# Kernel tuning notes

Measured on AMD Instinct MI355X. Metric: run time of the kernel, lower is better.

## Reference

```python
import jax, jax.numpy as jnp
import numpy as np

N_MET = 100000
N_RXN = 200000
E_SUB = 400000
E_PROD = 400000
HIDDEN = 128
MSG_DIM = 64
DT = 0.01  # flux-limited Euler step


def setup_inputs() -> dict:
    key = jax.random.key(0)
    ks = jax.random.split(key, 16)
    inp = {
        "x": jax.random.uniform(ks[0], (N_MET, 8), dtype=jnp.float32),
        "met_sub": jax.random.randint(ks[1], (E_SUB,), 0, N_MET, dtype=jnp.int32),
        "rxn_sub": jax.random.randint(ks[2], (E_SUB,), 0, N_RXN, dtype=jnp.int32),
        "sto_sub": jax.random.uniform(ks[3], (E_SUB,), dtype=jnp.float32) + 0.5,
        "met_prod": jax.random.randint(ks[4], (E_PROD,), 0, N_MET, dtype=jnp.int32),
        "rxn_prod": jax.random.randint(ks[5], (E_PROD,), 0, N_RXN, dtype=jnp.int32),
        "sto_prod": jax.random.uniform(ks[6], (E_PROD,), dtype=jnp.float32) + 0.5,
        # msg_mlp: Linear(2->HIDDEN), Tanh, Linear(HIDDEN->MSG_DIM)
        "W1": jax.random.normal(ks[7], (2, HIDDEN), dtype=jnp.float32) * 0.5,
        "b1": jnp.zeros((HIDDEN,), dtype=jnp.float32),
        "W2": jax.random.normal(ks[8], (HIDDEN, MSG_DIM), dtype=jnp.float32) * (1.0 / np.sqrt(HIDDEN)),
        "b2": jnp.zeros((MSG_DIM,), dtype=jnp.float32),
        # rate_mlp: Linear(MSG_DIM->HIDDEN), Tanh, Linear(HIDDEN->1)
        "V1": jax.random.normal(ks[9], (MSG_DIM, HIDDEN), dtype=jnp.float32) * (1.0 / np.sqrt(MSG_DIM)),
        "c1": jnp.zeros((HIDDEN,), dtype=jnp.float32),
        "V2": jax.random.normal(ks[10], (HIDDEN, 1), dtype=jnp.float32) * (1.0 / np.sqrt(HIDDEN)),
        "c2": jnp.zeros((1,), dtype=jnp.float32),
        # log_k ~ U(-2, 1)
        "log_k": jax.random.uniform(ks[11], (N_RXN,), dtype=jnp.float32, minval=-2.0, maxval=1.0),
    }
    return inp


def reference(x, met_sub, rxn_sub, sto_sub, met_prod, rxn_prod, sto_prod,
              W1, b1, W2, b2, V1, c1, V2, c2, log_k):
    n_met = x.shape[0]
    n_rxn = log_k.shape[0]
    conc = x[:, 3]          # [n_met]
    ext = x[:, 4]           # [n_met]

    # gather substrate concentrations -> per-edge msg MLP
    x_src = conc[met_sub]                                   # [E_sub]
    msg_in = jnp.stack([x_src, sto_sub], axis=-1)           # [E_sub, 2]
    h = jnp.tanh(msg_in @ W1 + b1)                          # [E_sub, HIDDEN]
    msg = h @ W2 + b2                                       # [E_sub, MSG_DIM]

    # scatter-add into per-reaction accumulators
    h_rxn = jax.ops.segment_sum(msg, rxn_sub, num_segments=n_rxn)  # [n_rxn, MSG_DIM]

    k = jnp.power(10.0, log_k)                              # [n_rxn]
    base_v = jax.nn.softplus((jnp.tanh(h_rxn @ V1 + c1) @ V2 + c2)[:, 0])  # [n_rxn]

    # multiplicative_substrate modulation: mean external input over substrates
    ones_e = jnp.ones_like(sto_sub)
    n_sub_per_rxn = jnp.clip(jax.ops.segment_sum(ones_e, rxn_sub, num_segments=n_rxn), 1.0)
    ext_agg = jax.ops.segment_sum(ext[met_sub], rxn_sub, num_segments=n_rxn)
    ext_mean = ext_agg / n_sub_per_rxn
    v = k * ext_mean * base_v                               # [n_rxn]

    # flux limiting (dt > 0): no substrate over-consumed in one Euler step
    consumption = sto_sub * v[rxn_sub] * DT                 # [E_sub]
    total_consumption = jax.ops.segment_sum(consumption, met_sub, num_segments=n_met)
    active = total_consumption > 1e-12
    safe_tot = jnp.where(active, total_consumption, 1.0)
    met_scale = jnp.where(active, jnp.minimum(conc / safe_tot, 1.0), 1.0)
    edge_scale = met_scale[met_sub]
    rxn_scale = jnp.ones((n_rxn,), dtype=v.dtype).at[rxn_sub].min(edge_scale)
    v = v * rxn_scale

    # scatter stoichiometric contributions back to metabolites
    met_all = jnp.concatenate([met_sub, met_prod])
    rxn_all = jnp.concatenate([rxn_sub, rxn_prod])
    sto_all = jnp.concatenate([-sto_sub, sto_prod])         # substrates negative, products positive
    contrib = sto_all * v[rxn_all]                          # [E_all]
    dxdt = jax.ops.segment_sum(contrib, met_all, num_segments=n_met)
    return dxdt[:, None]                                    # [n_met, 1]
```

## Files before the change

### kernel.cpp

```cpp
#include <hip/hip_runtime.h>
#include <hip/hip_fp16.h>
#include <cmath>
#include <cstdint>

#define N_MET   100000
#define N_RXN   200000
#define E_SUB   400000
#define E_PROD  400000
#define HIDDEN  128
#define MSG_DIM 64
#define DT      0.01f
#define TGRID   16
#define TGP     17
#define NPTS    (TGP * TGP)
#define CCH     16
#define RPB     128
#define RSB     512
#define NGRP    ((N_RXN + RPB - 1) / RPB)
#define CAP     8
#define OVFMAX  4096
#define NBS8    ((E_SUB / 8 + 255) / 256)
#define PBLK    ((E_PROD + RSB * 4 - 1) / (RSB * 4))
#define STK     10

typedef _Float16 h2v __attribute__((ext_vector_type(2)));

__device__ __forceinline__ float dot2f(uint32_t a, uint32_t b, float c) {
#if __has_builtin(__builtin_amdgcn_fdot2)
    return __builtin_amdgcn_fdot2(__builtin_bit_cast(h2v, a),
                                  __builtin_bit_cast(h2v, b), c, false);
#else
    float2 fa = __half22float2(*(__half2*)&a);
    float2 fb = __half22float2(*(__half2*)&b);
    return fmaf(fa.x, fb.x, fmaf(fa.y, fb.y, c));
#endif
}

__device__ __forceinline__ float fast_tanh(float x) {
    float t = __expf(2.0f * x);
    return 1.0f - 2.0f * __builtin_amdgcn_rcpf(t + 1.0f);
}

__device__ __forceinline__ float softplus_f(float x) {
    return (x > 20.0f) ? x : log1pf(__expf(x));
}

__global__ void __launch_bounds__(256)
prep_all(const float* __restrict__ W1, const float* __restrict__ b1,
         const float* __restrict__ W2, const float* __restrict__ b2,
         const float* __restrict__ V1, __half* __restrict__ TGh,
         const int* __restrict__ rxn_sub, const int* __restrict__ met_sub,
         const float* __restrict__ sto_sub, const float* __restrict__ x,
         int* __restrict__ cnt,
         uint4* __restrict__ recs,
         uint4* __restrict__ ovf, uint2* __restrict__ ovf2,
         int* __restrict__ ovf_cnt) {
    __shared__ float h_s[HIDDEN];
    __shared__ float msg_s[MSG_DIM];
    int bid = blockIdx.x;
    int tid = threadIdx.x;
    if (bid < NPTS) {
        int p = bid;
        int ia = p / TGP, ib = p % TGP;
        float a = (float)ia * (1.0f / TGRID);
        float b = 0.5f + (float)ib * (1.0f / TGRID);
        if (tid < HIDDEN)
            h_s[tid] = tanhf(fmaf(a, W1[tid], fmaf(b, W1[HIDDEN + tid], b1[tid])));
        __syncthreads();
        if (tid < MSG_DIM) {
            float acc = b2[tid];
            #pragma unroll 4
            for (int j = 0; j < HIDDEN; ++j)
                acc = fmaf(h_s[j], W2[j * MSG_DIM + tid], acc);
            msg_s[tid] = acc;
        }
        __syncthreads();
        if (tid < HIDDEN) {
            float g = 0.0f;
            #pragma unroll 4
            for (int m = 0; m < MSG_DIM; ++m)
                g = fmaf(msg_s[m], V1[m * HIDDEN + tid], g);
            int c = tid >> 3;
            int h = tid & 7;
            TGh[((size_t)(c * NPTS + p) * 8) + h] = __float2half(g);
        }
        return;
    }
    int i8 = (bid - NPTS) * 256 + tid;
    if (i8 >= E_SUB / 8) return;
    int4   rr0 = ((const int4*)rxn_sub)[2 * i8],     rr1 = ((const int4*)rxn_sub)[2 * i8 + 1];
    int4   mm0 = ((const int4*)met_sub)[2 * i8],     mm1 = ((const int4*)met_sub)[2 * i8 + 1];
    float4 ss0 = ((const float4*)sto_sub)[2 * i8],   ss1 = ((const float4*)sto_sub)[2 * i8 + 1];
    #pragma unroll
    for (int u = 0; u < 8; ++u) {
        int r  = (u < 4) ? (&rr0.x)[u] : (&rr1.x)[u - 4];
        int me = (u < 4) ? (&mm0.x)[u] : (&mm1.x)[u - 4];
        float se  = (u < 4) ? (&ss0.x)[u] : (&ss1.x)[u - 4];
        float ae  = x[me * 8 + 3];
        float ext = x[me * 8 + 4];
        float fa = ae * (float)TGRID;
        float fb = (se - 0.5f) * (float)TGRID;
        int ia = (int)fa; ia = ia < 0 ? 0 : (ia > TGRID - 1 ? TGRID - 1 : ia);
        int ib = (int)fb; ib = ib < 0 ? 0 : (ib > TGRID - 1 ? TGRID - 1 : ib);
        float wa = fa - (float)ia, wb = fb - (float)ib;
        float ua = 1.0f - wa, ub = 1.0f - wb;
        __half2 hA = __floats2half2_rn(ua * ub, ua * wb);
        __half2 hB = __floats2half2_rn(wa * ub, wa * wb);
        __half2 hS = __floats2half2_rn(se, ext);
        int cell = ia * TGP + ib;
        int slot = atomicAdd(&cnt[r], 1);
        uint4 rec;
        rec.y = *(uint32_t*)&hA;
        rec.z = *(uint32_t*)&hB;
        rec.w = *(uint32_t*)&hS;
        if (slot < CAP) {
            rec.x = (uint32_t)cell | ((uint32_t)me << 10);
            recs[(size_t)r * CAP + slot] = rec;
        } else {
            int o = atomicAdd(ovf_cnt, 1);
            if (o < OVFMAX) {
                rec.x = (uint32_t)cell | ((uint32_t)r << 10);
                ovf[o] = rec;
                ovf2[o] = make_uint2((uint32_t)me, 0u);
            }
        }
    }
}

__global__ void __launch_bounds__(RSB, 4)
rxn_quad(const int* __restrict__ cnt, const uint4* __restrict__ recs,
         const uint4* __restrict__ ovf, const uint2* __restrict__ ovf2,
         const int* __restrict__ ovf_cnt, const uint32_t* __restrict__ TG,
         const float* __restrict__ c1, const float* __restrict__ V2,
         const float* __restrict__ c2, const float* __restrict__ log_k,
         const int* __restrict__ rxn_prod, const int* __restrict__ met_prod,
         const float* __restrict__ sto_prod,
         int* __restrict__ pcnt, uint2* __restrict__ precs,
         uint4* __restrict__ povf, int* __restrict__ povf_cnt,
         float* __restrict__ v_out, float* __restrict__ tot) {
    __shared__ uint4 tbl4[CCH * NPTS];
    __shared__ float c1s[HIDDEN];
    __shared__ float v2s[HIDDEN];
    __shared__ int sorted_s[RPB];
    __shared__ int h16[16];
    int t = threadIdx.x;
    if (blockIdx.x < PBLK) {
        int i4 = blockIdx.x * RSB + t;
        if (i4 >= E_PROD / 4) return;
        int4   rr = ((const int4*)rxn_prod)[i4];
        int4   mm = ((const int4*)met_prod)[i4];
        float4 ss = ((const float4*)sto_prod)[i4];
        #pragma unroll
        for (int u = 0; u < 4; ++u) {
            int r  = (&rr.x)[u];
            int me = (&mm.x)[u];
            float sp = (&ss.x)[u];
            int slot = atomicAdd(&pcnt[r], 1);
            if (slot < CAP) {
                precs[(size_t)r * CAP + slot] = make_uint2((uint32_t)me, __float_as_uint(sp));
            } else {
                int o = atomicAdd(povf_cnt, 1);
                if (o < OVFMAX)
                    povf[o] = make_uint4((uint32_t)r, (uint32_t)me, __float_as_uint(sp), 0u);
            }
        }
        return;
    }
    int rbase = (blockIdx.x - PBLK) * RPB;
    int nval = N_RXN - rbase; if (nval > RPB) nval = RPB;

    const uint4* src = (const uint4*)TG;
    uint4 st[STK];
    #pragma unroll
    for (int k = 0; k < STK; ++k) {
        int i = t + k * RSB;
        if (i < CCH * NPTS) st[k] = src[i];
    }

    if (t < 16) h16[t] = 0;
    if (t < HIDDEN) { c1s[t] = c1[t]; v2s[t] = V2[t]; }
    __syncthreads();
    int n1 = -1, k1 = 0;
    if (t < nval) {
        n1 = cnt[rbase + t];
        k1 = n1 > 15 ? 15 : n1;
        atomicAdd(&h16[k1], 1);
    }
    __syncthreads();
    if (t == 0) {
        int acc = 0;
        #pragma unroll
        for (int b = 0; b < 16; ++b) { int c = h16[b]; h16[b] = acc; acc += c; }
    }
    __syncthreads();
    if (n1 >= 0) sorted_s[atomicAdd(&h16[k1], 1)] = t;

    #pragma unroll
    for (int k = 0; k < STK; ++k) {
        int i = t + k * RSB;
        if (i < CCH * NPTS) tbl4[i] = st[k];
    }
    __syncthreads();

    int slot = t >> 2, q = t & 3;
    if (slot >= nval) return;
    int r = rbase + sorted_s[slot];
    int n = cnt[r];
    int nmain = n < CAP ? n : CAP;
    float z[32];
    #pragma unroll
    for (int cc = 0; cc < 4; ++cc)
        #pragma unroll
        for (int s = 0; s < 8; ++s)
            z[cc * 8 + s] = c1s[(q + 4 * cc) * 8 + s];
    float eacc = 0.0f;
    const uint4* rrec = recs + (size_t)r * CAP;
    for (int e = 0; e < nmain; ++e) {
        uint4 rec = rrec[e];
        int cell = (int)(rec.x & 1023);
        float2 sx = __half22float2(*(__half2*)&rec.w);
        eacc += sx.y;
        #pragma unroll
        for (int cc = 0; cc < 4; ++cc) {
            const uint4* base = tbl4 + (q + 4 * cc) * NPTS + cell;
            uint4 A = base[0];
            uint4 B = base[1];
            uint4 C = base[TGP];
            uint4 D = base[TGP + 1];
            #pragma unroll
            for (int u = 0; u < 4; ++u) {
                uint32_t au = (&A.x)[u], bu = (&B.x)[u], cu = (&C.x)[u], du = (&D.x)[u];
                uint32_t ab0 = __builtin_amdgcn_perm(bu, au, 0x05040100u);
                uint32_t ab1 = __builtin_amdgcn_perm(bu, au, 0x07060302u);
                uint32_t cd0 = __builtin_amdgcn_perm(du, cu, 0x05040100u);
                uint32_t cd1 = __builtin_amdgcn_perm(du, cu, 0x07060302u);
                int j = cc * 8 + 2 * u;
                z[j]     = dot2f(ab0, rec.y, dot2f(cd0, rec.z, z[j]));
                z[j + 1] = dot2f(ab1, rec.y, dot2f(cd1, rec.z, z[j + 1]));
            }
        }
    }
    int oc = 0;
    if (n > CAP) {
        oc = *ovf_cnt; if (oc > OVFMAX) oc = OVFMAX;
        for (int o = 0; o < oc; ++o) {
            uint4 rec = ovf[o];
            if ((int)(rec.x >> 10) != r) continue;
            int cell = (int)(rec.x & 1023);
            float2 sx = __half22float2(*(__half2*)&rec.w);
            eacc += sx.y;
            #pragma unroll
            for (int cc = 0; cc < 4; ++cc) {
                const uint4* base = tbl4 + (q + 4 * cc) * NPTS + cell;
                uint4 A = base[0];
                uint4 B = base[1];
                uint4 C = base[TGP];
                uint4 D = base[TGP + 1];
                #pragma unroll
                for (int u = 0; u < 4; ++u) {
                    uint32_t au = (&A.x)[u], bu = (&B.x)[u], cu = (&C.x)[u], du = (&D.x)[u];
                    uint32_t ab0 = __builtin_amdgcn_perm(bu, au, 0x05040100u);
                    uint32_t ab1 = __builtin_amdgcn_perm(bu, au, 0x07060302u);
                    uint32_t cd0 = __builtin_amdgcn_perm(du, cu, 0x05040100u);
                    uint32_t cd1 = __builtin_amdgcn_perm(du, cu, 0x07060302u);
                    int j = cc * 8 + 2 * u;
                    z[j]     = dot2f(ab0, rec.y, dot2f(cd0, rec.z, z[j]));
                    z[j + 1] = dot2f(ab1, rec.y, dot2f(cd1, rec.z, z[j + 1]));
                }
            }
        }
    }
    float pp = 0.0f;
    #pragma unroll
    for (int cc = 0; cc < 4; ++cc)
        #pragma unroll
        for (int s = 0; s < 8; ++s)
            pp = fmaf(v2s[(q + 4 * cc) * 8 + s], fast_tanh(z[cc * 8 + s]), pp);
    pp += __shfl_xor(pp, 1);
    pp += __shfl_xor(pp, 2);
    float em = eacc / (float)(n > 0 ? n : 1);
    float bv = softplus_f(pp + c2[0]);
    float k  = __expf(log_k[r] * 2.302585092994046f);
    float vr = k * em * bv;
    if (q == 0) v_out[r] = vr;
    float w = vr * DT;
    for (int e = q; e < nmain; e += 4) {
        uint4 rec = rrec[e];
        float2 sx = __half22float2(*(__half2*)&rec.w);
        atomicAdd(&tot[rec.x >> 10], sx.x * w);
    }
    if (n > CAP && q == 0) {
        for (int o = 0; o < oc; ++o) {
            if ((int)(ovf[o].x >> 10) != r) continue;
            float2 sx = __half22float2(*(__half2*)&ovf[o].w);
            atomicAdd(&tot[ovf2[o].x], sx.x * w);
        }
    }
}

__global__ void __launch_bounds__(256)
scale8(const int* __restrict__ cnt, const int* __restrict__ pcnt,
       const uint4* __restrict__ recs, const uint2* __restrict__ precs,
       const uint4* __restrict__ ovf, const uint2* __restrict__ ovf2,
       const uint4* __restrict__ povf,
       const int* __restrict__ ovf_cnt, const int* __restrict__ povf_cnt,
       const float* __restrict__ x, const float* __restrict__ tot,
       const float* __restrict__ v, float* __restrict__ out) {
    int t = blockIdx.x * blockDim.x + threadIdx.x;
    int r = t >> 3, l = t & 7;
    if (r >= N_RXN) return;
    int n = cnt[r];
    int nmain = n < CAP ? n : CAP;
    uint4 rec = recs[(size_t)r * CAP + l];
    uint32_t m = rec.x >> 10;
    float sto = 0.0f;
    float cand = 1.0f;
    if (l < nmain) {
        float2 sx = __half22float2(*(__half2*)&rec.w);
        sto = sx.x;
        float tc = tot[m];
        if (tc > 1e-12f) cand = fminf(x[m * 8 + 3] / tc, 1.0f);
    }
    int oc = 0;
    if (n > CAP) {
        oc = *ovf_cnt; if (oc > OVFMAX) oc = OVFMAX;
        if (l == 0) {
            for (int o = 0; o < oc; ++o) {
                if ((int)(ovf[o].x >> 10) != r) continue;
                uint32_t mm = ovf2[o].x;
                float tc = tot[mm];
                if (tc > 1e-12f) cand = fminf(cand, fminf(x[mm * 8 + 3] / tc, 1.0f));
            }
        }
    }
    cand = fminf(cand, __shfl_xor(cand, 1));
    cand = fminf(cand, __shfl_xor(cand, 2));
    cand = fminf(cand, __shfl_xor(cand, 4));
    float vr = v[r] * cand;
    if (l < nmain) atomicAdd(&out[m], -sto * vr);
    if (n > CAP && l == 0) {
        for (int o = 0; o < oc; ++o) {
            if ((int)(ovf[o].x >> 10) != r) continue;
            float2 sx = __half22float2(*(__half2*)&ovf[o].w);
            atomicAdd(&out[ovf2[o].x], -sx.x * vr);
        }
    }
    int np = pcnt[r];
    int npm = np < CAP ? np : CAP;
    if (l < npm) {
        uint2 pr = precs[(size_t)r * CAP + l];
        atomicAdd(&out[pr.x], __uint_as_float(pr.y) * vr);
    }
    if (np > CAP && l == 0) {
        int oc2 = *povf_cnt; if (oc2 > OVFMAX) oc2 = OVFMAX;
        for (int o = 0; o < oc2; ++o) {
            if ((int)povf[o].x != r) continue;
            atomicAdd(&out[povf[o].y], __uint_as_float(povf[o].z) * vr);
        }
    }
}

extern "C" void kernel_launch(void* const* d_in, const int* in_sizes, int n_in,
                              void* d_out, int out_size, void* d_ws, size_t ws_size,
                              hipStream_t stream) {
    const float* x        = (const float*)d_in[0];
    const int*   met_sub  = (const int*)d_in[1];
    const int*   rxn_sub  = (const int*)d_in[2];
    const float* sto_sub  = (const float*)d_in[3];
    const int*   met_prod = (const int*)d_in[4];
    const int*   rxn_prod = (const int*)d_in[5];
    const float* sto_prod = (const float*)d_in[6];
    const float* W1       = (const float*)d_in[7];
    const float* b1       = (const float*)d_in[8];
    const float* W2       = (const float*)d_in[9];
    const float* b2       = (const float*)d_in[10];
    const float* V1       = (const float*)d_in[11];
    const float* c1       = (const float*)d_in[12];
    const float* V2       = (const float*)d_in[13];
    const float* c2       = (const float*)d_in[14];
    const float* log_k    = (const float*)d_in[15];

    uint4* recs    = (uint4*)d_ws;
    uint2* precs   = (uint2*)(recs + (size_t)N_RXN * CAP);
    uint4* ovf     = (uint4*)(precs + (size_t)N_RXN * CAP);
    uint2* ovf2    = (uint2*)(ovf + OVFMAX);
    uint4* povf    = (uint4*)(ovf2 + OVFMAX);
    int*   cnt     = (int*)(povf + OVFMAX);
    int*   pcnt    = cnt + N_RXN;
    float* tot     = (float*)(pcnt + N_RXN);
    int*   ovf_cnt = (int*)(tot + N_MET);
    int*   povf_cnt = ovf_cnt + 1;
    float* v       = (float*)(povf_cnt + 3);
    uint32_t* TG   = (uint32_t*)(v + N_RXN);
    float* outf = (float*)d_out;

    size_t zbytes = (size_t)(2 * N_RXN + N_MET + 4) * 4;
    hipMemsetAsync(cnt, 0, zbytes, stream);
    hipMemsetAsync(outf, 0, (size_t)N_MET * 4, stream);

    prep_all<<<NPTS + NBS8, 256, 0, stream>>>(
        W1, b1, W2, b2, V1, (__half*)TG,
        rxn_sub, met_sub, sto_sub, x,
        cnt, recs, ovf, ovf2, ovf_cnt);
    rxn_quad<<<PBLK + NGRP, RSB, 0, stream>>>(
        cnt, recs, ovf, ovf2, ovf_cnt, TG,
        c1, V2, c2, log_k,
        rxn_prod, met_prod, sto_prod,
        pcnt, precs, povf, povf_cnt,
        v, tot);
    scale8<<<((size_t)N_RXN * 8 + 255) / 256, 256, 0, stream>>>(
        cnt, pcnt, recs, precs, ovf, ovf2, povf, ovf_cnt, povf_cnt,
        x, tot, v, outf);
}
```

Measured before the change: 259.6 us.

## Split LDS table into two half-hidden passes to raise occupancy

Halves the shared-memory lookup table by loading eight hidden chunks at a time and processing the hidden dimension in two passes, each with a 16-register accumulator instead of 32. The register staging of the table is dropped and launch bounds go from 4 to 6 blocks per CU. The aim is more resident waves to hide LDS and gather latency. In exchange, each thread re-reads its edge records in both passes and the block adds an extra table load and barrier. The PBLK formula is rewritten but yields the same value.

```diff
diff --git a/kernel.cpp b/kernel.cpp
--- a/kernel.cpp
+++ b/kernel.cpp
@@ -14,14 +14,14 @@
 #define TGP     17
 #define NPTS    (TGP * TGP)
 #define CCH     16
+#define HCH     8
 #define RPB     128
 #define RSB     512
 #define NGRP    ((N_RXN + RPB - 1) / RPB)
 #define CAP     8
 #define OVFMAX  4096
 #define NBS8    ((E_SUB / 8 + 255) / 256)
-#define PBLK    ((E_PROD + RSB * 4 - 1) / (RSB * 4))
-#define STK     10
+#define PBLK    ((E_PROD / 4 + RSB - 1) / RSB)
 
 typedef _Float16 h2v __attribute__((ext_vector_type(2)));
 
@@ -127,7 +127,7 @@
     }
 }
 
-__global__ void __launch_bounds__(RSB, 4)
+__global__ void __launch_bounds__(RSB, 6)
 rxn_quad(const int* __restrict__ cnt, const uint4* __restrict__ recs,
          const uint4* __restrict__ ovf, const uint2* __restrict__ ovf2,
          const int* __restrict__ ovf_cnt, const uint32_t* __restrict__ TG,
@@ -138,7 +138,7 @@
          int* __restrict__ pcnt, uint2* __restrict__ precs,
          uint4* __restrict__ povf, int* __restrict__ povf_cnt,
          float* __restrict__ v_out, float* __restrict__ tot) {
-    __shared__ uint4 tbl4[CCH * NPTS];
+    __shared__ uint4 tbl4[HCH * NPTS];
     __shared__ float c1s[HIDDEN];
     __shared__ float v2s[HIDDEN];
     __shared__ int sorted_s[RPB];
@@ -169,14 +169,6 @@
     int rbase = (blockIdx.x - PBLK) * RPB;
     int nval = N_RXN - rbase; if (nval > RPB) nval = RPB;
 
-    const uint4* src = (const uint4*)TG;
-    uint4 st[STK];
-    #pragma unroll
-    for (int k = 0; k < STK; ++k) {
-        int i = t + k * RSB;
-        if (i < CCH * NPTS) st[k] = src[i];
-    }
-
     if (t < 16) h16[t] = 0;
     if (t < HIDDEN) { c1s[t] = c1[t]; v2s[t] = V2[t]; }
     __syncthreads();
@@ -195,87 +187,93 @@
     __syncthreads();
     if (n1 >= 0) sorted_s[atomicAdd(&h16[k1], 1)] = t;
 
-    #pragma unroll
-    for (int k = 0; k < STK; ++k) {
-        int i = t + k * RSB;
-        if (i < CCH * NPTS) tbl4[i] = st[k];
-    }
-    __syncthreads();
-
     int slot = t >> 2, q = t & 3;
-    if (slot >= nval) return;
-    int r = rbase + sorted_s[slot];
-    int n = cnt[r];
-    int nmain = n < CAP ? n : CAP;
-    float z[32];
-    #pragma unroll
-    for (int cc = 0; cc < 4; ++cc)
-        #pragma unroll
-        for (int s = 0; s < 8; ++s)
-            z[cc * 8 + s] = c1s[(q + 4 * cc) * 8 + s];
-    float eacc = 0.0f;
-    const uint4* rrec = recs + (size_t)r * CAP;
-    for (int e = 0; e < nmain; ++e) {
-        uint4 rec = rrec[e];
-        int cell = (int)(rec.x & 1023);
-        float2 sx = __half22float2(*(__half2*)&rec.w);
-        eacc += sx.y;
-        #pragma unroll
-        for (int cc = 0; cc < 4; ++cc) {
-            const uint4* base = tbl4 + (q + 4 * cc) * NPTS + cell;
-            uint4 A = base[0];
-            uint4 B = base[1];
-            uint4 C = base[TGP];
-            uint4 D = base[TGP + 1];
+    int r = -1, n = 0, nmain = 0, oc = 0;
+    const uint4* rrec = nullptr;
+    float pp = 0.0f, eacc = 0.0f;
+
+    #pragma unroll 1
+    for (int pass = 0; pass < 2; ++pass) {
+        if (pass) __syncthreads();
+        {
+            const uint4* src = (const uint4*)TG + pass * (HCH * NPTS);
+            for (int i = t; i < HCH * NPTS; i += RSB) tbl4[i] = src[i];
+        }
+        __syncthreads();
+        if (pass == 0 && slot < nval) {
+            r = rbase + sorted_s[slot];
+            n = cnt[r];
+            nmain = n < CAP ? n : CAP;
+            rrec = recs + (size_t)r * CAP;
+        }
+        if (r >= 0) {
+            float z[16];
             #pragma unroll
-            for (int u = 0; u < 4; ++u) {
-                uint32_t au = (&A.x)[u], bu = (&B.x)[u], cu = (&C.x)[u], du = (&D.x)[u];
-                uint32_t ab0 = __builtin_amdgcn_perm(bu, au, 0x05040100u);
-                uint32_t ab1 = __builtin_amdgcn_perm(bu, au, 0x07060302u);
-                uint32_t cd0 = __builtin_amdgcn_perm(du, cu, 0x05040100u);
-                uint32_t cd1 = __builtin_amdgcn_perm(du, cu, 0x07060302u);
-                int j = cc * 8 + 2 * u;
-                z[j]     = dot2f(ab0, rec.y, dot2f(cd0, rec.z, z[j]));
-                z[j + 1] = dot2f(ab1, rec.y, dot2f(cd1, rec.z, z[j + 1]));
-            }
-        }
-    }
-    int oc = 0;
-    if (n > CAP) {
-        oc = *ovf_cnt; if (oc > OVFMAX) oc = OVFMAX;
-        for (int o = 0; o < oc; ++o) {
-            uint4 rec = ovf[o];
-            if ((int)(rec.x >> 10) != r) continue;
-            int cell = (int)(rec.x & 1023);
-            float2 sx = __half22float2(*(__half2*)&rec.w);
-            eacc += sx.y;
-            #pragma unroll
-            for (int cc = 0; cc < 4; ++cc) {
-                const uint4* base = tbl4 + (q + 4 * cc) * NPTS + cell;
-                uint4 A = base[0];
-                uint4 B = base[1];
-                uint4 C = base[TGP];
-                uint4 D = base[TGP + 1];
+            for (int j = 0; j < 16; ++j) z[j] = c1s[pass * 64 + q * 16 + j];
+            for (int e = 0; e < nmain; ++e) {
+                uint4 rec = rrec[e];
+                int cell = (int)(rec.x & 1023);
+                if (pass == 0) {
+                    float2 sx = __half22float2(*(__half2*)&rec.w);
+                    eacc += sx.y;
+                }
                 #pragma unroll
-                for (int u = 0; u < 4; ++u) {
-                    uint32_t au = (&A.x)[u], bu = (&B.x)[u], cu = (&C.x)[u], du = (&D.x)[u];
-                    uint32_t ab0 = __builtin_amdgcn_perm(bu, au, 0x05040100u);
-                    uint32_t ab1 = __builtin_amdgcn_perm(bu, au, 0x07060302u);
-                    uint32_t cd0 = __builtin_amdgcn_perm(du, cu, 0x05040100u);
-                    uint32_t cd1 = __builtin_amdgcn_perm(du, cu, 0x07060302u);
-                    int j = cc * 8 + 2 * u;
-                    z[j]     = dot2f(ab0, rec.y, dot2f(cd0, rec.z, z[j]));
-                    z[j + 1] = dot2f(ab1, rec.y, dot2f(cd1, rec.z, z[j + 1]));
+                for (int lc2 = 0; lc2 < 2; ++lc2) {
+                    const uint4* base = tbl4 + (2 * q + lc2) * NPTS + cell;
+                    uint4 A = base[0];
+                    uint4 B = base[1];
+                    uint4 C = base[TGP];
+                    uint4 D = base[TGP + 1];
+                    #pragma unroll
+                    for (int u = 0; u < 4; ++u) {
+                        uint32_t au = (&A.x)[u], bu = (&B.x)[u], cu = (&C.x)[u], du = (&D.x)[u];
+                        uint32_t ab0 = __builtin_amdgcn_perm(bu, au, 0x05040100u);
+                        uint32_t ab1 = __builtin_amdgcn_perm(bu, au, 0x07060302u);
+                        uint32_t cd0 = __builtin_amdgcn_perm(du, cu, 0x05040100u);
+                        uint32_t cd1 = __builtin_amdgcn_perm(du, cu, 0x07060302u);
+                        int j = lc2 * 8 + 2 * u;
+                        z[j]     = dot2f(ab0, rec.y, dot2f(cd0, rec.z, z[j]));
+                        z[j + 1] = dot2f(ab1, rec.y, dot2f(cd1, rec.z, z[j + 1]));
+                    }
                 }
             }
-        }
-    }
-    float pp = 0.0f;
-    #pragma unroll
-    for (int cc = 0; cc < 4; ++cc)
-        #pragma unroll
-        for (int s = 0; s < 8; ++s)
-            pp = fmaf(v2s[(q + 4 * cc) * 8 + s], fast_tanh(z[cc * 8 + s]), pp);
+            if (n > CAP) {
+                if (pass == 0) { oc = *ovf_cnt; if (oc > OVFMAX) oc = OVFMAX; }
+                for (int o = 0; o < oc; ++o) {
+                    uint4 rec = ovf[o];
+                    if ((int)(rec.x >> 10) != r) continue;
+                    int cell = (int)(rec.x & 1023);
+                    if (pass == 0) {
+                        float2 sx = __half22float2(*(__half2*)&rec.w);
+                        eacc += sx.y;
+                    }
+                    #pragma unroll
+                    for (int lc2 = 0; lc2 < 2; ++lc2) {
+                        const uint4* base = tbl4 + (2 * q + lc2) * NPTS + cell;
+                        uint4 A = base[0];
+                        uint4 B = base[1];
+                        uint4 C = base[TGP];
+                        uint4 D = base[TGP + 1];
+                        #pragma unroll
+                        for (int u = 0; u < 4; ++u) {
+                            uint32_t au = (&A.x)[u], bu = (&B.x)[u], cu = (&C.x)[u], du = (&D.x)[u];
+                            uint32_t ab0 = __builtin_amdgcn_perm(bu, au, 0x05040100u);
+                            uint32_t ab1 = __builtin_amdgcn_perm(bu, au, 0x07060302u);
+                            uint32_t cd0 = __builtin_amdgcn_perm(du, cu, 0x05040100u);
+                            uint32_t cd1 = __builtin_amdgcn_perm(du, cu, 0x07060302u);
+                            int j = lc2 * 8 + 2 * u;
+                            z[j]     = dot2f(ab0, rec.y, dot2f(cd0, rec.z, z[j]));
+                            z[j + 1] = dot2f(ab1, rec.y, dot2f(cd1, rec.z, z[j + 1]));
+                        }
+                    }
+                }
+            }
+            #pragma unroll
+            for (int j = 0; j < 16; ++j)
+                pp = fmaf(v2s[pass * 64 + q * 16 + j], fast_tanh(z[j]), pp);
+        }
+    }
+    if (r < 0) return;
     pp += __shfl_xor(pp, 1);
     pp += __shfl_xor(pp, 2);
     float em = eacc / (float)(n > 0 ? n : 1);
```

Measured after the change: 223.6 us. -13.9%, faster.
